# Kernel tuning notes

Hardware: AMD Instinct MI355X
Metric: run time of the kernel (lower is better)

## Reference

```python
import jax, jax.numpy as jnp
import numpy as np

BS, NQ, NC = 128, 900, 91
PRE_TOPK = 10000      # source: pre_topk when n_queries*n_cls > 10000
POST_TOPK = 100       # source: keep_inds[:100]
IOU_THRESH = 0.7


def box_cxcywh_to_xyxy(b):
    cx, cy, w, h = b[..., 0], b[..., 1], b[..., 2], b[..., 3]
    return jnp.stack([cx - 0.5 * w, cy - 0.5 * h, cx + 0.5 * w, cy + 0.5 * h], axis=-1)


def nms_image(boxes, scores, labels):
    """Greedy batched NMS, returning the first POST_TOPK picked indices.
    boxes: [PRE,4] xyxy (scaled), scores: [PRE] desc-sorted, labels: [PRE] int.
    batched_nms trick: offset boxes per class so IoU across classes is 0."""
    max_coord = jnp.max(boxes)
    off = labels.astype(boxes.dtype) * (max_coord + 1.0)
    ob = boxes + off[:, None]                          # [PRE,4]
    areas = (ob[:, 2] - ob[:, 0]) * (ob[:, 3] - ob[:, 1])

    def step(active, _):
        s = jnp.where(active, scores, -jnp.inf)
        i = jnp.argmax(s)                              # highest-score surviving box
        bi = ob[i]
        xx1 = jnp.maximum(bi[0], ob[:, 0])
        yy1 = jnp.maximum(bi[1], ob[:, 1])
        xx2 = jnp.minimum(bi[2], ob[:, 2])
        yy2 = jnp.minimum(bi[3], ob[:, 3])
        inter = jnp.clip(xx2 - xx1, 0.0) * jnp.clip(yy2 - yy1, 0.0)
        union = areas[i] + areas - inter
        iou = inter / jnp.maximum(union, 1e-9)
        # suppress IoU > thresh (includes i itself since iou(i,i)=1)
        active = active & (iou <= IOU_THRESH)
        return active, i

    _, keep = jax.lax.scan(step, jnp.ones(ob.shape[0], dtype=bool), None, length=POST_TOPK)
    return keep                                         # [POST]


def setup_inputs() -> dict:
    key = jax.random.key(0)
    k1, k2, k3, k4 = jax.random.split(key, 4)
    pred_logits = jax.random.normal(k1, (BS, NQ, NC), dtype=jnp.float32) * 2.0 - 2.0
    cxcy = jax.random.uniform(k2, (BS, NQ, 2), dtype=jnp.float32)
    wh = jax.random.uniform(k3, (BS, NQ, 2), dtype=jnp.float32, minval=0.02, maxval=0.3)
    pred_boxes = jnp.concatenate([cxcy, wh], axis=-1)   # cxcywh in [0,1]
    target_sizes = jax.random.uniform(k4, (BS, 2), dtype=jnp.float32, minval=480.0, maxval=1333.0)
    return {"pred_logits": pred_logits, "pred_boxes": pred_boxes, "target_sizes": target_sizes}


def reference(pred_logits, pred_boxes, target_sizes):
    bs, nq, nc = pred_logits.shape
    prob = jax.nn.sigmoid(pred_logits).reshape(bs, nq * nc)      # all_scores
    boxes = box_cxcywh_to_xyxy(pred_boxes)                        # [bs,nq,4]
    img_h, img_w = target_sizes[:, 0], target_sizes[:, 1]
    scale = jnp.stack([img_w, img_h, img_w, img_h], axis=1)       # [bs,4]
    boxes = boxes * scale[:, None, :]

    top_scores, top_idx = jax.lax.top_k(prob, PRE_TOPK)           # [bs,PRE]
    top_labels = top_idx % nc                                     # all_labels gather
    top_box_idx = top_idx // nc                                   # all_boxes gather
    top_boxes = jnp.take_along_axis(boxes, top_box_idx[..., None], axis=1)  # [bs,PRE,4]

    keep = jax.vmap(nms_image)(top_boxes, top_scores, top_labels)  # [bs,POST]
    out_scores = jnp.take_along_axis(top_scores, keep, axis=1)
    out_labels = jnp.take_along_axis(top_labels, keep, axis=1)
    out_boxes = jnp.take_along_axis(top_boxes, keep[..., None], axis=1)
    return out_scores, out_labels, out_boxes
```

## Files before the change

kernel.cpp:

```cpp
#include <hip/hip_runtime.h>
#include <cstdint>

#pragma clang fp contract(off)

#define BS   128
#define NQ   900
#define NC   91
#define NQC  (NQ * NC)
#define Q4   (NQC / 4)
#define PRE  10000
#define POST 100
#define NCAP 12288
#define TBITS 13
#define TBINS (1 << TBITS)
#define TSHIFT (32 - TBITS)
#define K_WIN 16
#define HSEG 1024
#define KS   2780

typedef unsigned long long ull;

__device__ __forceinline__ uint32_t fkey(float f) {
    uint32_t b = __float_as_uint(f);
    return (b & 0x80000000u) ? ~b : (b | 0x80000000u);
}
__device__ __forceinline__ float unkey(uint32_t u) {
    uint32_t b = (u & 0x80000000u) ? (u & 0x7FFFFFFFu) : ~u;
    return __uint_as_float(b);
}
__device__ __forceinline__ uint32_t qclamp(uint32_t q) { return (q < NQ) ? q : (NQ - 1); }

__device__ __forceinline__ ull shflx(ull v, int j) {
    uint32_t lo = (uint32_t)__shfl_xor((int)(uint32_t)v, j, 64);
    uint32_t hi = (uint32_t)__shfl_xor((int)(uint32_t)(v >> 32), j, 64);
    return ((ull)hi << 32) | (ull)lo;
}
__device__ __forceinline__ ull cex(ull v, int j, bool lower, bool desc) {
    ull pb = shflx(v, j);
    ull a = lower ? v : pb;
    ull b = lower ? pb : v;
    bool sw = desc ? (a < b) : (a > b);
    return sw ? pb : v;
}
__device__ __forceinline__ void ce(ull& a, ull& b, bool desc) {
    bool sw = desc ? (a < b) : (a > b);
    if (sw) { ull t = a; a = b; b = t; }
}

__global__ void __launch_bounds__(1024) k_fused(const float* __restrict__ logits,
                                                const float* __restrict__ pred_boxes,
                                                const float* __restrict__ target_sizes,
                                                float* __restrict__ out) {
    const int img = blockIdx.x;
    const int tid = threadIdx.x;
    const int lane = tid & 63;
    const int wv = tid >> 6;

    __shared__ ull ca[NCAP];
    __shared__ float4 shPB[NQ];
    __shared__ ull binK[HSEG];
    __shared__ ull headK[HSEG];
    __shared__ uint32_t hist12[4096];
    __shared__ uint32_t part[1024];
    __shared__ float aX1[POST], aY1[POST], aX2[POST], aY2[POST], aAr[POST];
    __shared__ int   aCl[POST];
    __shared__ float s_x1[K_WIN], s_y1[K_WIN], s_x2[K_WIN], s_y2[K_WIN];
    __shared__ int   s_cl[K_WIN];
    __shared__ uint32_t s_em[K_WIN];
    __shared__ float sOffD;
    __shared__ ull sF0;
    __shared__ uint32_t sCnt, sCntA, sCntB, sTlo, sMX;
    __shared__ uint32_t sB1, sTp1, sB2, sTp2;

    uint32_t* hist13 = (uint32_t*)ca;

    const float ih = target_sizes[img * 2 + 0];
    const float iw = target_sizes[img * 2 + 1];
    const float* pb = pred_boxes + (size_t)img * NQ * 4;
    const float4* lg4 = (const float4*)(logits + (size_t)img * NQC);

    auto mckey = [&](uint32_t f) -> uint32_t {
        uint32_t q = qclamp(f / NC);
        float4 bb = shPB[q];
        float x1 = (bb.x - 0.5f * bb.z) * iw;
        float y1 = (bb.y - 0.5f * bb.w) * ih;
        float x2 = (bb.x + 0.5f * bb.z) * iw;
        float y2 = (bb.y + 0.5f * bb.w) * ih;
        return fkey(fmaxf(fmaxf(x1, y1), fmaxf(x2, y2)));
    };

    if (tid < NQ) shPB[tid] = ((const float4*)pb)[tid];
    for (int i = tid; i < TBINS; i += 1024) hist13[i] = 0u;
    for (int i = tid; i < 4096; i += 1024) hist12[i] = 0u;
    if (tid == 0) { sCnt = 0u; sMX = 0u; sF0 = 0ull; }
    float4 sv[5];
    #pragma unroll
    for (int c = 0; c < 5; ++c) sv[c] = lg4[c * 4096 + tid];
    __syncthreads();

    #pragma unroll
    for (int c = 0; c < 5; ++c) {
        atomicAdd(&hist13[fkey(sv[c].x) >> TSHIFT], 1u);
        atomicAdd(&hist13[fkey(sv[c].y) >> TSHIFT], 1u);
        atomicAdd(&hist13[fkey(sv[c].z) >> TSHIFT], 1u);
        atomicAdd(&hist13[fkey(sv[c].w) >> TSHIFT], 1u);
    }
    __syncthreads();
    {
        uint32_t s = 0;
        int b0 = tid * 8;
        #pragma unroll
        for (int j = 0; j < 8; ++j) s += hist13[b0 + j];
        part[tid] = s;
    }
    __syncthreads();
    if (tid < 64) {
        uint32_t pv[16]; uint32_t tot = 0;
        #pragma unroll
        for (int j = 0; j < 16; ++j) { pv[j] = part[tid * 16 + j]; tot += pv[j]; }
        uint32_t sinc = tot;
        #pragma unroll
        for (int off = 1; off < 64; off <<= 1) {
            uint32_t o = (uint32_t)__shfl_down((int)sinc, off, 64);
            if (tid + off < 64) sinc += o;
        }
        uint32_t cum = sinc - tot;
        for (int j = 15; j >= 0; --j) {
            if (cum < KS && cum + pv[j] >= KS) {
                int pbn = (tid * 16 + j) * 8;
                uint32_t c2 = cum;
                for (int b = pbn + 7; b >= pbn; --b) {
                    if (c2 + hist13[b] >= KS) { sTlo = ((uint32_t)b) << TSHIFT; break; }
                    c2 += hist13[b];
                }
            }
            cum += pv[j];
        }
    }
    __syncthreads();
    const uint32_t Tlo = sTlo;

    for (int i0 = 0; i0 < Q4; i0 += 1024) {
        int i = i0 + tid;
        bool inb = (i < Q4);
        float4 v = inb ? lg4[i] : make_float4(0.f, 0.f, 0.f, 0.f);
        uint32_t u0 = fkey(v.x), u1 = fkey(v.y), u2 = fkey(v.z), u3 = fkey(v.w);
        bool p0 = inb && u0 >= Tlo, p1 = inb && u1 >= Tlo;
        bool p2 = inb && u2 >= Tlo, p3 = inb && u3 >= Tlo;
        ull m0 = __ballot(p0), m1 = __ballot(p1), m2 = __ballot(p2), m3 = __ballot(p3);
        uint32_t c0 = (uint32_t)__popcll(m0), c1 = (uint32_t)__popcll(m1);
        uint32_t c2 = (uint32_t)__popcll(m2), c3 = (uint32_t)__popcll(m3);
        uint32_t wb = 0u;
        if (lane == 0) wb = atomicAdd(&sCnt, c0 + c1 + c2 + c3);
        wb = (uint32_t)__shfl((int)wb, 0, 64);
        ull lm = (1ull << lane) - 1ull;
        uint32_t fi = (uint32_t)(i * 4);
        uint32_t b0 = wb + (uint32_t)__popcll(m0 & lm);
        uint32_t b1 = wb + c0 + (uint32_t)__popcll(m1 & lm);
        uint32_t b2 = wb + c0 + c1 + (uint32_t)__popcll(m2 & lm);
        uint32_t b3 = wb + c0 + c1 + c2 + (uint32_t)__popcll(m3 & lm);
        if (p0) { if (b0 < NCAP) ca[b0] = ((ull)u0 << 32) | (ull)(0xFFFFFFFFu - (fi + 0)); atomicAdd(&hist12[u0 >> 20], 1u); }
        if (p1) { if (b1 < NCAP) ca[b1] = ((ull)u1 << 32) | (ull)(0xFFFFFFFFu - (fi + 1)); atomicAdd(&hist12[u1 >> 20], 1u); }
        if (p2) { if (b2 < NCAP) ca[b2] = ((ull)u2 << 32) | (ull)(0xFFFFFFFFu - (fi + 2)); atomicAdd(&hist12[u2 >> 20], 1u); }
        if (p3) { if (b3 < NCAP) ca[b3] = ((ull)u3 << 32) | (ull)(0xFFFFFFFFu - (fi + 3)); atomicAdd(&hist12[u3 >> 20], 1u); }
    }
    __syncthreads();
    const uint32_t cnt = (sCnt < NCAP) ? sCnt : NCAP;
    const uint32_t TK = (cnt < PRE) ? cnt : PRE;
    const uint32_t T2 = (TK < HSEG) ? TK : HSEG;

    {
        int b0 = tid * 4;
        part[tid] = hist12[b0] + hist12[b0 + 1] + hist12[b0 + 2] + hist12[b0 + 3];
        binK[tid] = 0ull; headK[tid] = 0ull;
        if (tid == 0) { sCntA = 0u; sCntB = 0u; }
    }
    __syncthreads();
    if (tid < 64) {
        uint32_t pv[16]; uint32_t tot = 0;
        #pragma unroll
        for (int j = 0; j < 16; ++j) { pv[j] = part[tid * 16 + j]; tot += pv[j]; }
        uint32_t sinc = tot;
        #pragma unroll
        for (int off = 1; off < 64; off <<= 1) {
            uint32_t o = (uint32_t)__shfl_down((int)sinc, off, 64);
            if (tid + off < 64) sinc += o;
        }
        uint32_t cum = sinc - tot;
        for (int j = 15; j >= 0; --j) {
            if (cum < TK && cum + pv[j] >= TK) {
                int pbn = (tid * 16 + j) * 4;
                uint32_t c2 = cum;
                for (int b = pbn + 3; b >= pbn; --b) {
                    if (c2 + hist12[b] >= TK) { sB1 = (uint32_t)b; sTp1 = TK - c2; break; }
                    c2 += hist12[b];
                }
            }
            if (cum < T2 && cum + pv[j] >= T2) {
                int pbn = (tid * 16 + j) * 4;
                uint32_t c2 = cum;
                for (int b = pbn + 3; b >= pbn; --b) {
                    if (c2 + hist12[b] >= T2) { sB2 = (uint32_t)b; sTp2 = T2 - c2; break; }
                    c2 += hist12[b];
                }
            }
            cum += pv[j];
        }
    }
    __syncthreads();
    const uint32_t B1 = sB1, tp1 = sTp1;
    const uint32_t B2 = sB2;
    const int C1 = (int)(T2 - sTp2);

    uint32_t lmx = 0u;
    {
        const int rounds = (int)((cnt + 1023u) >> 10);
        for (int r = 0; r < rounds; ++r) {
            int i = tid + (r << 10);
            bool live = (i < (int)cnt);
            ull x = live ? ca[i] : 0ull;
            uint32_t bin = (uint32_t)(x >> 52);
            if (live && bin > B1) {
                uint32_t km = mckey(~(uint32_t)x);
                if (km > lmx) lmx = km;
            }
            bool isA = live && (bin == B1);
            bool isB = live && (bin > B2);
            ull mA = __ballot(isA), mB = __ballot(isB);
            uint32_t wbA = 0u, wbB = 0u;
            if (lane == 0) {
                uint32_t cA = (uint32_t)__popcll(mA), cB = (uint32_t)__popcll(mB);
                if (cA) wbA = atomicAdd(&sCntA, cA);
                if (cB) wbB = atomicAdd(&sCntB, cB);
            }
            wbA = (uint32_t)__shfl((int)wbA, 0, 64);
            wbB = (uint32_t)__shfl((int)wbB, 0, 64);
            ull lm = (1ull << lane) - 1ull;
            if (isA) { uint32_t p = wbA + (uint32_t)__popcll(mA & lm); if (p < HSEG) binK[p] = x; }
            if (isB) { uint32_t p = wbB + (uint32_t)__popcll(mB & lm); if (p < HSEG) headK[p] = x; }
        }
    }
    __syncthreads();

    {
        ull r0 = 0, r1 = 0, r2 = 0, r3 = 0;
        const int cw = wv & 3;
        const int cb = cw << 8;
        ull* A = (wv < 4) ? binK : headK;
        if (wv < 8) {
            r0 = A[cb | lane]; r1 = A[cb | 64 | lane];
            r2 = A[cb | 128 | lane]; r3 = A[cb | 192 | lane];
            #pragma unroll
            for (int k2 = 2; k2 <= 32; k2 <<= 1) {
                bool d = ((lane & k2) == 0);
                #pragma unroll
                for (int j = 16; j >= 1; j >>= 1) {
                    if (j <= (k2 >> 1)) {
                        bool lw = ((lane & j) == 0);
                        r0 = cex(r0, j, lw, d); r1 = cex(r1, j, lw, d);
                        r2 = cex(r2, j, lw, d); r3 = cex(r3, j, lw, d);
                    }
                }
            }
            #pragma unroll
            for (int j = 32; j >= 1; j >>= 1) {
                bool lw = ((lane & j) == 0);
                r0 = cex(r0, j, lw, true);  r1 = cex(r1, j, lw, false);
                r2 = cex(r2, j, lw, true);  r3 = cex(r3, j, lw, false);
            }
            ce(r0, r1, true); ce(r2, r3, false);
            #pragma unroll
            for (int j = 32; j >= 1; j >>= 1) {
                bool lw = ((lane & j) == 0);
                r0 = cex(r0, j, lw, true);  r1 = cex(r1, j, lw, true);
                r2 = cex(r2, j, lw, false); r3 = cex(r3, j, lw, false);
            }
            {
                bool d = ((cw & 1) == 0);
                ce(r0, r2, d); ce(r1, r3, d); ce(r0, r1, d); ce(r2, r3, d);
                #pragma unroll
                for (int j = 32; j >= 1; j >>= 1) {
                    bool lw = ((lane & j) == 0);
                    r0 = cex(r0, j, lw, d); r1 = cex(r1, j, lw, d);
                    r2 = cex(r2, j, lw, d); r3 = cex(r3, j, lw, d);
                }
            }
            A[cb | lane] = r0; A[cb | 64 | lane] = r1;
            A[cb | 128 | lane] = r2; A[cb | 192 | lane] = r3;
        }
        __syncthreads();
        {
            ull* Bp = (tid >> 9) ? headK : binK;
            int t = tid & 511;
            int i = ((t & ~255) << 1) | (t & 255);
            int ixj = i | 256;
            bool d = ((i & 512) == 0);
            ull a = Bp[i], b = Bp[ixj];
            bool sw = d ? (a < b) : (a > b);
            if (sw) { Bp[i] = b; Bp[ixj] = a; }
        }
        __syncthreads();
        if (wv < 8) {
            r0 = A[cb | lane]; r1 = A[cb | 64 | lane];
            r2 = A[cb | 128 | lane]; r3 = A[cb | 192 | lane];
            bool d = ((cw & 2) == 0);
            ce(r0, r2, d); ce(r1, r3, d); ce(r0, r1, d); ce(r2, r3, d);
            #pragma unroll
            for (int j = 32; j >= 1; j >>= 1) {
                bool lw = ((lane & j) == 0);
                r0 = cex(r0, j, lw, d); r1 = cex(r1, j, lw, d);
                r2 = cex(r2, j, lw, d); r3 = cex(r3, j, lw, d);
            }
            A[cb | lane] = r0; A[cb | 64 | lane] = r1;
            A[cb | 128 | lane] = r2; A[cb | 192 | lane] = r3;
        }
        __syncthreads();
        {
            ull* Bp = (tid >> 9) ? headK : binK;
            int t = tid & 511;
            ull a = Bp[t], b = Bp[t | 512];
            if (a < b) { Bp[t] = b; Bp[t | 512] = a; }
        }
        __syncthreads();
        {
            ull* Bp = (tid >> 9) ? headK : binK;
            int t = tid & 511;
            int i = ((t & ~255) << 1) | (t & 255);
            int ixj = i | 256;
            ull a = Bp[i], b = Bp[ixj];
            if (a < b) { Bp[i] = b; Bp[ixj] = a; }
        }
        __syncthreads();
        if (wv < 8) {
            r0 = A[cb | lane]; r1 = A[cb | 64 | lane];
            r2 = A[cb | 128 | lane]; r3 = A[cb | 192 | lane];
            ce(r0, r2, true); ce(r1, r3, true); ce(r0, r1, true); ce(r2, r3, true);
            #pragma unroll
            for (int j = 32; j >= 1; j >>= 1) {
                bool lw = ((lane & j) == 0);
                r0 = cex(r0, j, lw, true); r1 = cex(r1, j, lw, true);
                r2 = cex(r2, j, lw, true); r3 = cex(r3, j, lw, true);
            }
            A[cb | lane] = r0; A[cb | 64 | lane] = r1;
            A[cb | 128 | lane] = r2; A[cb | 192 | lane] = r3;
        }
        __syncthreads();
    }

    if (tid < (int)tp1) {
        ull x = binK[tid];
        if (x != 0ull) { uint32_t km = mckey(~(uint32_t)x); if (km > lmx) lmx = km; }
    }
    for (int off = 32; off > 0; off >>= 1) {
        uint32_t o = (uint32_t)__shfl_down((int)lmx, off, 64);
        if (o > lmx) lmx = o;
    }
    if (lane == 0) atomicMax(&sMX, lmx);
    if (tid == 0 && C1 > 0) sF0 = headK[0];
    __syncthreads();
    float offD;
    {
        uint32_t m = sMX;
        uint32_t b = (m & 0x80000000u) ? (m & 0x7FFFFFFFu) : ~m;
        offD = __uint_as_float(b) + 1.0f;
    }

    auto sort1024 = [&]() {
        const int idx = tid;
        ull x = headK[idx];
        #pragma unroll
        for (int k2 = 2; k2 <= 32; k2 <<= 1) {
            bool d = ((lane & k2) == 0);
            #pragma unroll
            for (int j = 16; j >= 1; j >>= 1)
                if (j <= (k2 >> 1)) x = cex(x, j, (lane & j) == 0, d);
        }
        {
            bool d = ((idx & 64) == 0);
            #pragma unroll
            for (int j = 32; j >= 1; j >>= 1) x = cex(x, j, (lane & j) == 0, d);
        }
        for (int k = 128; k <= 1024; k <<= 1) {
            headK[idx] = x;
            __syncthreads();
            for (int j = k >> 1; j >= 64; j >>= 1) {
                if (tid < 512) {
                    int i2 = ((tid & ~(j - 1)) << 1) | (tid & (j - 1));
                    int ixj = i2 | j;
                    ull a = headK[i2], b = headK[ixj];
                    bool sw = ((i2 & k) == 0) ? (a < b) : (a > b);
                    if (sw) { headK[i2] = b; headK[ixj] = a; }
                }
                __syncthreads();
            }
            x = headK[idx];
            bool d = ((idx & k) == 0);
            #pragma unroll
            for (int j = 32; j >= 1; j >>= 1) x = cex(x, j, (lane & j) == 0, d);
        }
        headK[idx] = x;
        __syncthreads();
    };

    int npick = 0, base = 0, segbase = 0, segend = C1;
    int bcur = (int)B2;
    bool needF0 = (C1 == 0);
    while (npick < POST) {
        if (base >= segend) {
            if (segend >= (int)TK) {
                ull x0 = sF0;
                uint32_t f0 = ~(uint32_t)x0;
                uint32_t u0 = (uint32_t)(x0 >> 32);
                uint32_t q0 = qclamp(f0 / NC);
                uint32_t c0 = f0 - (f0 / NC) * NC;
                float4 bb = shPB[q0];
                float rx1 = (bb.x - 0.5f * bb.z) * iw;
                float ry1 = (bb.y - 0.5f * bb.w) * ih;
                float rx2 = (bb.x + 0.5f * bb.z) * iw;
                float ry2 = (bb.y + 0.5f * bb.w) * ih;
                float sc = 1.0f / (1.0f + expf(-unkey(u0)));
                for (int p2 = npick + tid; p2 < POST; p2 += 1024) {
                    out[img * POST + p2] = sc;
                    out[BS * POST + img * POST + p2] = (float)c0;
                    float* ob2 = out + 2 * BS * POST + ((size_t)img * POST + p2) * 4;
                    ob2[0] = rx1; ob2[1] = ry1; ob2[2] = rx2; ob2[3] = ry2;
                }
                break;
            }
            while (bcur > 0 && hist12[bcur] == 0u) --bcur;
            headK[tid] = 0ull;
            if (tid == 0) sCntA = 0u;
            __syncthreads();
            {
                const int rounds = (int)((cnt + 1023u) >> 10);
                for (int r2 = 0; r2 < rounds; ++r2) {
                    int i = tid + (r2 << 10);
                    bool pass = (i < (int)cnt) && ((uint32_t)(ca[i] >> 52) == (uint32_t)bcur);
                    ull x = pass ? ca[i] : 0ull;
                    ull m = __ballot(pass);
                    uint32_t below = (uint32_t)__popcll(m & ((1ull << lane) - 1ull));
                    uint32_t wtot = (uint32_t)__popcll(m);
                    uint32_t wb = 0u;
                    if (lane == 0 && wtot) wb = atomicAdd(&sCntA, wtot);
                    wb = (uint32_t)__shfl((int)wb, 0, 64);
                    if (pass) { uint32_t p = wb + below; if (p < HSEG) headK[p] = x; }
                }
            }
            __syncthreads();
            sort1024();
            int avail = (int)((sCntA < (uint32_t)HSEG) ? sCntA : (uint32_t)HSEG);
            int take = (int)TK - segend; if (take > avail) take = avail;
            if (needF0) { if (tid == 0) sF0 = headK[0]; needF0 = false; __syncthreads(); }
            segbase = segend; segend += take; --bcur;
            continue;
        }

        const int r = base + wv;
        const bool val = (r < segend);
        const ull xk = headK[val ? (r - segbase) : 0];
        const uint32_t f = val ? ~(uint32_t)xk : 0u;
        const uint32_t uk = (uint32_t)(xk >> 32);
        const uint32_t q = qclamp(f / NC);
        const uint32_t cc = f - (f / NC) * NC;
        float4 bb = shPB[q];
        const float x1 = (bb.x - 0.5f * bb.z) * iw;
        const float y1 = (bb.y - 0.5f * bb.w) * ih;
        const float x2 = (bb.x + 0.5f * bb.z) * iw;
        const float y2 = (bb.y + 0.5f * bb.w) * ih;
        if (lane == 0) {
            s_x1[wv] = x1; s_y1[wv] = y1; s_x2[wv] = x2; s_y2[wv] = y2;
            s_cl[wv] = val ? (int)cc : -1;
        }
        __syncthreads();

        const float o = (float)cc * offD;
        const float cx1 = x1 + o, cy1 = y1 + o, cx2 = x2 + o, cy2 = y2 + o;
        const float car = (cx2 - cx1) * (cy2 - cy1);
        bool cf = false;
        if (val && lane < wv && s_cl[lane] == (int)cc) {
            float jx1 = s_x1[lane] + o, jy1 = s_y1[lane] + o;
            float jx2 = s_x2[lane] + o, jy2 = s_y2[lane] + o;
            float arj = (jx2 - jx1) * (jy2 - jy1);
            float xx1 = fmaxf(jx1, cx1), yy1 = fmaxf(jy1, cy1);
            float xx2 = fminf(jx2, cx2), yy2 = fminf(jy2, cy2);
            float inter = fmaxf(xx2 - xx1, 0.0f) * fmaxf(yy2 - yy1, 0.0f);
            float uni = (arj + car) - inter;
            float iou = inter / fmaxf(uni, 1e-9f);
            cf = !(iou <= 0.7f);
        }
        uint32_t em = (uint32_t)(__ballot(cf) & 0xFFFFull);
        bool pf = false;
        for (int i2 = lane; i2 < npick; i2 += 64) {
            if (aCl[i2] == (int)cc) {
                float jx1 = aX1[i2] + o, jy1 = aY1[i2] + o;
                float jx2 = aX2[i2] + o, jy2 = aY2[i2] + o;
                float arj = aAr[i2];
                float xx1 = fmaxf(jx1, cx1), yy1 = fmaxf(jy1, cy1);
                float xx2 = fminf(jx2, cx2), yy2 = fminf(jy2, cy2);
                float inter = fmaxf(xx2 - xx1, 0.0f) * fmaxf(yy2 - yy1, 0.0f);
                float uni = (arj + car) - inter;
                float iou = inter / fmaxf(uni, 1e-9f);
                pf |= !(iou <= 0.7f);
            }
        }
        bool anyPrior = (__ballot(pf) != 0ull);
        if (lane == 0)
            s_em[wv] = em | (anyPrior ? 0x80000000u : 0u) | (val ? 0u : 0x40000000u);
        __syncthreads();

        uint32_t acc = 0u; int a = 0;
        const int room = POST - npick;
        #pragma unroll
        for (int w2 = 0; w2 < K_WIN; ++w2) {
            uint32_t ew = s_em[w2];
            if (!(ew & 0xC0000000u) && a < room && ((ew & 0xFFFFu & acc) == 0u)) {
                acc |= (1u << w2); ++a;
            }
        }

        if (((acc >> wv) & 1u) && lane == 0) {
            int p = npick + __popc(acc & ((1u << wv) - 1u));
            float sc = 1.0f / (1.0f + expf(-unkey(uk)));
            out[img * POST + p] = sc;
            out[BS * POST + img * POST + p] = (float)cc;
            float* ob2 = out + 2 * BS * POST + ((size_t)img * POST + p) * 4;
            ob2[0] = x1; ob2[1] = y1; ob2[2] = x2; ob2[3] = y2;
            aX1[p] = x1; aY1[p] = y1; aX2[p] = x2; aY2[p] = y2;
            aAr[p] = car; aCl[p] = (int)cc;
        }
        npick += a;
        base += K_WIN;
    }
}

extern "C" void kernel_launch(void* const* d_in, const int* in_sizes, int n_in,
                              void* d_out, int out_size, void* d_ws, size_t ws_size,
                              hipStream_t stream) {
    const float* logits = (const float*)d_in[0];
    const float* boxes  = (const float*)d_in[1];
    const float* tsizes = (const float*)d_in[2];
    float* out = (float*)d_out;
    (void)d_ws; (void)ws_size;

    k_fused<<<BS, 1024, 0, stream>>>(logits, boxes, tsizes, out);
}
```

Measured before the change: 138.0 us.

## Split top-k selection into two-block histogram kernel plus selection kernel

```diff
diff --git a/kernel.cpp b/kernel.cpp
--- a/kernel.cpp
+++ b/kernel.cpp
@@ -8,9 +8,9 @@
 #define NC   91
 #define NQC  (NQ * NC)
 #define Q4   (NQC / 4)
+#define HHALF 10238
 #define PRE  10000
 #define POST 100
-#define NCAP 12288
 #define TBITS 13
 #define TBINS (1 << TBITS)
 #define TSHIFT (32 - TBITS)
@@ -20,6 +20,8 @@
 
 typedef unsigned long long ull;
 
+#define WS_GH 0
+
 __device__ __forceinline__ uint32_t fkey(float f) {
     uint32_t b = __float_as_uint(f);
     return (b & 0x80000000u) ? ~b : (b | 0x80000000u);
@@ -47,32 +49,112 @@
     if (sw) { ull t = a; a = b; b = t; }
 }
 
-__global__ void __launch_bounds__(1024) k_fused(const float* __restrict__ logits,
-                                                const float* __restrict__ pred_boxes,
-                                                const float* __restrict__ target_sizes,
-                                                float* __restrict__ out) {
+__global__ void __launch_bounds__(1024) k_hist(const float* __restrict__ logits,
+                                               uint16_t* __restrict__ ghist) {
+    const int img = blockIdx.x >> 1;
+    const int h = blockIdx.x & 1;
+    const int tid = threadIdx.x;
+    __shared__ uint32_t hist[TBINS];
+    __shared__ uint32_t part[1024];
+    __shared__ uint32_t sTB;
+    const float4* lg4 = (const float4*)(logits + (size_t)img * NQC);
+    for (int i = tid; i < TBINS; i += 1024) hist[i] = 0u;
+    float4 sv[5];
+    #pragma unroll
+    for (int c = 0; c < 5; ++c) sv[c] = lg4[c * 4096 + tid];
+    __syncthreads();
+    #pragma unroll
+    for (int c = 0; c < 5; ++c) {
+        atomicAdd(&hist[fkey(sv[c].x) >> TSHIFT], 1u);
+        atomicAdd(&hist[fkey(sv[c].y) >> TSHIFT], 1u);
+        atomicAdd(&hist[fkey(sv[c].z) >> TSHIFT], 1u);
+        atomicAdd(&hist[fkey(sv[c].w) >> TSHIFT], 1u);
+    }
+    __syncthreads();
+    {
+        uint32_t s = 0;
+        int b0 = tid * 8;
+        #pragma unroll
+        for (int j = 0; j < 8; ++j) s += hist[b0 + j];
+        part[tid] = s;
+    }
+    __syncthreads();
+    if (tid < 64) {
+        uint32_t pv[16]; uint32_t tot = 0;
+        #pragma unroll
+        for (int j = 0; j < 16; ++j) { pv[j] = part[tid * 16 + j]; tot += pv[j]; }
+        uint32_t sinc = tot;
+        #pragma unroll
+        for (int off = 1; off < 64; off <<= 1) {
+            uint32_t o = (uint32_t)__shfl_down((int)sinc, off, 64);
+            if (tid + off < 64) sinc += o;
+        }
+        uint32_t cum = sinc - tot;
+        for (int j = 15; j >= 0; --j) {
+            if (cum < KS && cum + pv[j] >= KS) {
+                int pbn = (tid * 16 + j) * 8;
+                uint32_t c2 = cum;
+                for (int b = pbn + 7; b >= pbn; --b) {
+                    if (c2 + hist[b] >= KS) { sTB = (uint32_t)b; break; }
+                    c2 += hist[b];
+                }
+            }
+            cum += pv[j];
+        }
+    }
+    __syncthreads();
+    const uint32_t TB = sTB;
+    for (int i = tid; i < TBINS; i += 1024) hist[i] = 0u;
+    __syncthreads();
+    const int lo = h * HHALF;
+    const int hi = (lo + HHALF < Q4) ? (lo + HHALF) : Q4;
+    for (int i0 = lo; i0 < hi; i0 += 4096) {
+        float4 v[4]; bool lv[4];
+        #pragma unroll
+        for (int s = 0; s < 4; ++s) {
+            int i = i0 + (s << 10) + tid;
+            lv[s] = (i < hi);
+            v[s] = lv[s] ? lg4[i] : make_float4(0.f, 0.f, 0.f, 0.f);
+        }
+        #pragma unroll
+        for (int s = 0; s < 4; ++s) {
+            if (lv[s]) {
+                uint32_t u;
+                u = fkey(v[s].x); if ((u >> TSHIFT) >= TB) atomicAdd(&hist[u >> TSHIFT], 1u);
+                u = fkey(v[s].y); if ((u >> TSHIFT) >= TB) atomicAdd(&hist[u >> TSHIFT], 1u);
+                u = fkey(v[s].z); if ((u >> TSHIFT) >= TB) atomicAdd(&hist[u >> TSHIFT], 1u);
+                u = fkey(v[s].w); if ((u >> TSHIFT) >= TB) atomicAdd(&hist[u >> TSHIFT], 1u);
+            }
+        }
+    }
+    __syncthreads();
+    uint16_t* g = ghist + (size_t)(img * 2 + h) * TBINS;
+    for (int i = tid; i < TBINS; i += 1024) g[i] = (uint16_t)hist[i];
+}
+
+__global__ void __launch_bounds__(1024) k_sel(const float* __restrict__ logits,
+                                              const uint16_t* __restrict__ ghist,
+                                              const float* __restrict__ pred_boxes,
+                                              const float* __restrict__ target_sizes,
+                                              float* __restrict__ out) {
     const int img = blockIdx.x;
     const int tid = threadIdx.x;
     const int lane = tid & 63;
     const int wv = tid >> 6;
 
-    __shared__ ull ca[NCAP];
+    __shared__ uint32_t hist[TBINS];
+    __shared__ uint32_t part[1024];
     __shared__ float4 shPB[NQ];
     __shared__ ull binK[HSEG];
     __shared__ ull headK[HSEG];
-    __shared__ uint32_t hist12[4096];
-    __shared__ uint32_t part[1024];
     __shared__ float aX1[POST], aY1[POST], aX2[POST], aY2[POST], aAr[POST];
     __shared__ int   aCl[POST];
     __shared__ float s_x1[K_WIN], s_y1[K_WIN], s_x2[K_WIN], s_y2[K_WIN];
     __shared__ int   s_cl[K_WIN];
     __shared__ uint32_t s_em[K_WIN];
-    __shared__ float sOffD;
     __shared__ ull sF0;
-    __shared__ uint32_t sCnt, sCntA, sCntB, sTlo, sMX;
-    __shared__ uint32_t sB1, sTp1, sB2, sTp2;
-
-    uint32_t* hist13 = (uint32_t*)ca;
+    __shared__ uint32_t sCntA, sCntB, sMX;
+    __shared__ uint32_t sB1, sTp1, sB2, sTp2, sTK;
 
     const float ih = target_sizes[img * 2 + 0];
     const float iw = target_sizes[img * 2 + 1];
@@ -90,30 +172,25 @@
     };
 
     if (tid < NQ) shPB[tid] = ((const float4*)pb)[tid];
-    for (int i = tid; i < TBINS; i += 1024) hist13[i] = 0u;
-    for (int i = tid; i < 4096; i += 1024) hist12[i] = 0u;
-    if (tid == 0) { sCnt = 0u; sMX = 0u; sF0 = 0ull; }
-    float4 sv[5];
-    #pragma unroll
-    for (int c = 0; c < 5; ++c) sv[c] = lg4[c * 4096 + tid];
-    __syncthreads();
-
-    #pragma unroll
-    for (int c = 0; c < 5; ++c) {
-        atomicAdd(&hist13[fkey(sv[c].x) >> TSHIFT], 1u);
-        atomicAdd(&hist13[fkey(sv[c].y) >> TSHIFT], 1u);
-        atomicAdd(&hist13[fkey(sv[c].z) >> TSHIFT], 1u);
-        atomicAdd(&hist13[fkey(sv[c].w) >> TSHIFT], 1u);
-    }
+    {
+        const uint16_t* g0 = ghist + (size_t)(img * 2) * TBINS;
+        const uint16_t* g1 = g0 + TBINS;
+        for (int i = tid; i < TBINS; i += 1024)
+            hist[i] = (uint32_t)g0[i] + (uint32_t)g1[i];
+    }
+    binK[tid] = 0ull; headK[tid] = 0ull;
+    if (tid == 0) { sCntA = 0u; sCntB = 0u; sMX = 0u; sF0 = 0ull;
+                    sB1 = 0u; sTp1 = 1u; sB2 = 0u; sTp2 = 0u; sTK = 0u; }
     __syncthreads();
     {
         uint32_t s = 0;
         int b0 = tid * 8;
         #pragma unroll
-        for (int j = 0; j < 8; ++j) s += hist13[b0 + j];
+        for (int j = 0; j < 8; ++j) s += hist[b0 + j];
         part[tid] = s;
     }
     __syncthreads();
+
     if (tid < 64) {
         uint32_t pv[16]; uint32_t tot = 0;
         #pragma unroll
@@ -124,120 +201,79 @@
             uint32_t o = (uint32_t)__shfl_down((int)sinc, off, 64);
             if (tid + off < 64) sinc += o;
         }
+        uint32_t total = (uint32_t)__shfl((int)sinc, 0, 64);
+        uint32_t TKl = (total < PRE) ? total : PRE;
+        uint32_t T2l = (TKl < HSEG) ? TKl : HSEG;
+        if (tid == 0) sTK = TKl;
         uint32_t cum = sinc - tot;
         for (int j = 15; j >= 0; --j) {
-            if (cum < KS && cum + pv[j] >= KS) {
+            if (cum < TKl && cum + pv[j] >= TKl) {
                 int pbn = (tid * 16 + j) * 8;
                 uint32_t c2 = cum;
                 for (int b = pbn + 7; b >= pbn; --b) {
-                    if (c2 + hist13[b] >= KS) { sTlo = ((uint32_t)b) << TSHIFT; break; }
-                    c2 += hist13[b];
+                    if (c2 + hist[b] >= TKl) { sB1 = (uint32_t)b; sTp1 = TKl - c2; break; }
+                    c2 += hist[b];
+                }
+            }
+            if (cum < T2l && cum + pv[j] >= T2l) {
+                int pbn = (tid * 16 + j) * 8;
+                uint32_t c2 = cum;
+                for (int b = pbn + 3 + 4; b >= pbn; --b) {
+                    if (c2 + hist[b] >= T2l) { sB2 = (uint32_t)b; sTp2 = T2l - c2; break; }
+                    c2 += hist[b];
                 }
             }
             cum += pv[j];
         }
     }
     __syncthreads();
-    const uint32_t Tlo = sTlo;
-
-    for (int i0 = 0; i0 < Q4; i0 += 1024) {
-        int i = i0 + tid;
-        bool inb = (i < Q4);
-        float4 v = inb ? lg4[i] : make_float4(0.f, 0.f, 0.f, 0.f);
-        uint32_t u0 = fkey(v.x), u1 = fkey(v.y), u2 = fkey(v.z), u3 = fkey(v.w);
-        bool p0 = inb && u0 >= Tlo, p1 = inb && u1 >= Tlo;
-        bool p2 = inb && u2 >= Tlo, p3 = inb && u3 >= Tlo;
-        ull m0 = __ballot(p0), m1 = __ballot(p1), m2 = __ballot(p2), m3 = __ballot(p3);
-        uint32_t c0 = (uint32_t)__popcll(m0), c1 = (uint32_t)__popcll(m1);
-        uint32_t c2 = (uint32_t)__popcll(m2), c3 = (uint32_t)__popcll(m3);
-        uint32_t wb = 0u;
-        if (lane == 0) wb = atomicAdd(&sCnt, c0 + c1 + c2 + c3);
-        wb = (uint32_t)__shfl((int)wb, 0, 64);
-        ull lm = (1ull << lane) - 1ull;
-        uint32_t fi = (uint32_t)(i * 4);
-        uint32_t b0 = wb + (uint32_t)__popcll(m0 & lm);
-        uint32_t b1 = wb + c0 + (uint32_t)__popcll(m1 & lm);
-        uint32_t b2 = wb + c0 + c1 + (uint32_t)__popcll(m2 & lm);
-        uint32_t b3 = wb + c0 + c1 + c2 + (uint32_t)__popcll(m3 & lm);
-        if (p0) { if (b0 < NCAP) ca[b0] = ((ull)u0 << 32) | (ull)(0xFFFFFFFFu - (fi + 0)); atomicAdd(&hist12[u0 >> 20], 1u); }
-        if (p1) { if (b1 < NCAP) ca[b1] = ((ull)u1 << 32) | (ull)(0xFFFFFFFFu - (fi + 1)); atomicAdd(&hist12[u1 >> 20], 1u); }
-        if (p2) { if (b2 < NCAP) ca[b2] = ((ull)u2 << 32) | (ull)(0xFFFFFFFFu - (fi + 2)); atomicAdd(&hist12[u2 >> 20], 1u); }
-        if (p3) { if (b3 < NCAP) ca[b3] = ((ull)u3 << 32) | (ull)(0xFFFFFFFFu - (fi + 3)); atomicAdd(&hist12[u3 >> 20], 1u); }
-    }
-    __syncthreads();
-    const uint32_t cnt = (sCnt < NCAP) ? sCnt : NCAP;
-    const uint32_t TK = (cnt < PRE) ? cnt : PRE;
-    const uint32_t T2 = (TK < HSEG) ? TK : HSEG;
-
-    {
-        int b0 = tid * 4;
-        part[tid] = hist12[b0] + hist12[b0 + 1] + hist12[b0 + 2] + hist12[b0 + 3];
-        binK[tid] = 0ull; headK[tid] = 0ull;
-        if (tid == 0) { sCntA = 0u; sCntB = 0u; }
-    }
-    __syncthreads();
-    if (tid < 64) {
-        uint32_t pv[16]; uint32_t tot = 0;
-        #pragma unroll
-        for (int j = 0; j < 16; ++j) { pv[j] = part[tid * 16 + j]; tot += pv[j]; }
-        uint32_t sinc = tot;
-        #pragma unroll
-        for (int off = 1; off < 64; off <<= 1) {
-            uint32_t o = (uint32_t)__shfl_down((int)sinc, off, 64);
-            if (tid + off < 64) sinc += o;
-        }
-        uint32_t cum = sinc - tot;
-        for (int j = 15; j >= 0; --j) {
-            if (cum < TK && cum + pv[j] >= TK) {
-                int pbn = (tid * 16 + j) * 4;
-                uint32_t c2 = cum;
-                for (int b = pbn + 3; b >= pbn; --b) {
-                    if (c2 + hist12[b] >= TK) { sB1 = (uint32_t)b; sTp1 = TK - c2; break; }
-                    c2 += hist12[b];
-                }
-            }
-            if (cum < T2 && cum + pv[j] >= T2) {
-                int pbn = (tid * 16 + j) * 4;
-                uint32_t c2 = cum;
-                for (int b = pbn + 3; b >= pbn; --b) {
-                    if (c2 + hist12[b] >= T2) { sB2 = (uint32_t)b; sTp2 = T2 - c2; break; }
-                    c2 += hist12[b];
-                }
-            }
-            cum += pv[j];
-        }
-    }
-    __syncthreads();
-    const uint32_t B1 = sB1, tp1 = sTp1;
-    const uint32_t B2 = sB2;
-    const int C1 = (int)(T2 - sTp2);
+    const uint32_t B1 = sB1, tp1 = sTp1, B2 = sB2;
+    const uint32_t TK = sTK;
+    const int C1 = (int)(((TK < (uint32_t)HSEG) ? TK : (uint32_t)HSEG) - sTp2);
 
     uint32_t lmx = 0u;
-    {
-        const int rounds = (int)((cnt + 1023u) >> 10);
-        for (int r = 0; r < rounds; ++r) {
-            int i = tid + (r << 10);
-            bool live = (i < (int)cnt);
-            ull x = live ? ca[i] : 0ull;
-            uint32_t bin = (uint32_t)(x >> 52);
-            if (live && bin > B1) {
-                uint32_t km = mckey(~(uint32_t)x);
-                if (km > lmx) lmx = km;
-            }
-            bool isA = live && (bin == B1);
-            bool isB = live && (bin > B2);
-            ull mA = __ballot(isA), mB = __ballot(isB);
-            uint32_t wbA = 0u, wbB = 0u;
-            if (lane == 0) {
-                uint32_t cA = (uint32_t)__popcll(mA), cB = (uint32_t)__popcll(mB);
-                if (cA) wbA = atomicAdd(&sCntA, cA);
-                if (cB) wbB = atomicAdd(&sCntB, cB);
-            }
-            wbA = (uint32_t)__shfl((int)wbA, 0, 64);
-            wbB = (uint32_t)__shfl((int)wbB, 0, 64);
-            ull lm = (1ull << lane) - 1ull;
-            if (isA) { uint32_t p = wbA + (uint32_t)__popcll(mA & lm); if (p < HSEG) binK[p] = x; }
-            if (isB) { uint32_t p = wbB + (uint32_t)__popcll(mB & lm); if (p < HSEG) headK[p] = x; }
+    for (int i0 = 0; i0 < Q4; i0 += 4096) {
+        float4 v[4]; int ib[4];
+        #pragma unroll
+        for (int s = 0; s < 4; ++s) {
+            int i = i0 + (s << 10) + tid;
+            ib[s] = i;
+            v[s] = (i < Q4) ? lg4[i] : make_float4(0.f, 0.f, 0.f, 0.f);
+        }
+        #pragma unroll
+        for (int s = 0; s < 4; ++s) {
+            const bool live = (ib[s] < Q4);
+            float comp[4] = {v[s].x, v[s].y, v[s].z, v[s].w};
+            #pragma unroll
+            for (int c = 0; c < 4; ++c) {
+                uint32_t u = fkey(comp[c]);
+                uint32_t bin = u >> TSHIFT;
+                uint32_t fi = (uint32_t)(ib[s] * 4 + c);
+                if (live && bin > B1) { uint32_t km = mckey(fi); if (km > lmx) lmx = km; }
+                bool isA = live && (bin == B1);
+                bool isB = live && (bin > B2);
+                ull key = ((ull)u << 32) | (ull)(0xFFFFFFFFu - fi);
+                ull mA = __ballot(isA);
+                if (mA) {
+                    uint32_t wb = 0u;
+                    if (lane == 0) wb = atomicAdd(&sCntA, (uint32_t)__popcll(mA));
+                    wb = (uint32_t)__shfl((int)wb, 0, 64);
+                    if (isA) {
+                        uint32_t p = wb + (uint32_t)__popcll(mA & ((1ull << lane) - 1ull));
+                        if (p < HSEG) binK[p] = key;
+                    }
+                }
+                ull mB = __ballot(isB);
+                if (mB) {
+                    uint32_t wb = 0u;
+                    if (lane == 0) wb = atomicAdd(&sCntB, (uint32_t)__popcll(mB));
+                    wb = (uint32_t)__shfl((int)wb, 0, 64);
+                    if (isB) {
+                        uint32_t p = wb + (uint32_t)__popcll(mB & ((1ull << lane) - 1ull));
+                        if (p < HSEG) headK[p] = key;
+                    }
+                }
+            }
         }
     }
     __syncthreads();
@@ -427,23 +463,30 @@
                 }
                 break;
             }
-            while (bcur > 0 && hist12[bcur] == 0u) --bcur;
+            while (bcur > 0 && hist[bcur] == 0u) --bcur;
             headK[tid] = 0ull;
             if (tid == 0) sCntA = 0u;
             __syncthreads();
-            {
-                const int rounds = (int)((cnt + 1023u) >> 10);
-                for (int r2 = 0; r2 < rounds; ++r2) {
-                    int i = tid + (r2 << 10);
-                    bool pass = (i < (int)cnt) && ((uint32_t)(ca[i] >> 52) == (uint32_t)bcur);
-                    ull x = pass ? ca[i] : 0ull;
+            for (int i0 = 0; i0 < Q4; i0 += 1024) {
+                int i = i0 + tid;
+                bool live = (i < Q4);
+                float4 v = live ? lg4[i] : make_float4(0.f, 0.f, 0.f, 0.f);
+                float comp[4] = {v.x, v.y, v.z, v.w};
+                #pragma unroll
+                for (int c = 0; c < 4; ++c) {
+                    uint32_t u = fkey(comp[c]);
+                    bool pass = live && ((u >> TSHIFT) == (uint32_t)bcur);
                     ull m = __ballot(pass);
-                    uint32_t below = (uint32_t)__popcll(m & ((1ull << lane) - 1ull));
-                    uint32_t wtot = (uint32_t)__popcll(m);
-                    uint32_t wb = 0u;
-                    if (lane == 0 && wtot) wb = atomicAdd(&sCntA, wtot);
-                    wb = (uint32_t)__shfl((int)wb, 0, 64);
-                    if (pass) { uint32_t p = wb + below; if (p < HSEG) headK[p] = x; }
+                    if (m) {
+                        uint32_t wb = 0u;
+                        if (lane == 0) wb = atomicAdd(&sCntA, (uint32_t)__popcll(m));
+                        wb = (uint32_t)__shfl((int)wb, 0, 64);
+                        if (pass) {
+                            uint32_t p = wb + (uint32_t)__popcll(m & ((1ull << lane) - 1ull));
+                            uint32_t fi = (uint32_t)(i * 4 + c);
+                            if (p < HSEG) headK[p] = ((ull)u << 32) | (ull)(0xFFFFFFFFu - fi);
+                        }
+                    }
                 }
             }
             __syncthreads();
@@ -540,7 +583,9 @@
     const float* boxes  = (const float*)d_in[1];
     const float* tsizes = (const float*)d_in[2];
     float* out = (float*)d_out;
-    (void)d_ws; (void)ws_size;
-
-    k_fused<<<BS, 1024, 0, stream>>>(logits, boxes, tsizes, out);
-}
+
+    uint16_t* ghist = (uint16_t*)((char*)d_ws + WS_GH);
+
+    k_hist<<<2 * BS, 1024, 0, stream>>>(logits, ghist);
+    k_sel<<<BS, 1024, 0, stream>>>(logits, ghist, boxes, tsizes, out);
+}
```

Measured after the change: 153.4 us. 11.2% more time.
